# Kernel tuning notes

Measured on AMD Instinct MI355X. Metric: run time of the kernel, lower is better.

Reference implementation:

```python
import jax, jax.numpy as jnp
import numpy as np
from jax import lax

ALPHA = 4.0  # spikingjelly default sigmoid surrogate alpha

@jax.custom_vjp
def spike(x):
    return (x >= 0.0).astype(x.dtype)

def _spike_fwd(x):
    return spike(x), x

def _spike_bwd(x, g):
    s = jax.nn.sigmoid(ALPHA * x)
    return (g * ALPHA * s * (1.0 - s),)

spike.defvjp(_spike_fwd, _spike_bwd)

def lif(x_seq, v_th=1.0, tau=2.0):
    # MultiStepLIFNode, v_reset=0, detach_reset=True, hard reset.
    def step(v, xt):
        v = v + (xt - v) / tau            # neuronal charge
        s = spike(v - v_th)               # fire
        v = v * (1.0 - lax.stop_gradient(s))  # detached hard reset to 0
        return v, s
    _, out = lax.scan(step, jnp.zeros_like(x_seq[0]), x_seq)
    return out

def bn(x, g, b, m, var, eps=1e-5):
    # BatchNorm1d inference over channel axis 2 of (T,B,C,N)
    inv = g / jnp.sqrt(var + eps)
    return x * inv[None, None, :, None] + (b - m * inv)[None, None, :, None]

def setup_inputs() -> dict:
    T, B, C, N = 4, 8, 512, 1024
    key = jax.random.key(0)
    ks = jax.random.split(key, 24)
    def w(k):  # 1x1 conv weight (C_out, C_in)
        return jax.random.normal(k, (C, C), jnp.float32) * (C ** -0.5)
    def bn_params(k):
        k1, k2, k3 = jax.random.split(k, 3)
        g = 1.0 + 0.1 * jax.random.normal(k1, (C,), jnp.float32)
        b = 0.1 * jax.random.normal(k2, (C,), jnp.float32)
        m = 0.1 * jax.random.normal(k3, (C,), jnp.float32)
        v = 0.5 + jax.random.uniform(jax.random.fold_in(k, 7), (C,), jnp.float32)
        return g, b, m, v
    gq, bq, mq, vq = bn_params(ks[1])
    gk, bk, mk, vk = bn_params(ks[3])
    gv, bv, mv, vv = bn_params(ks[5])
    gp, bp, mp, vp = bn_params(ks[7])
    return {
        'x': jax.random.normal(ks[0], (T, B, C, N), jnp.float32),
        'res_attn': jnp.zeros((1,), jnp.float32),
        'wq': w(ks[10]), 'gq': gq, 'bq': bq, 'mq': mq, 'vq': vq,
        'wk': w(ks[11]), 'gk': gk, 'bk': bk, 'mk': mk, 'vk': vk,
        'wv': w(ks[12]), 'gv': gv, 'bv': bv, 'mv': mv, 'vv': vv,
        'wp': w(ks[13]), 'pb': 0.1 * jax.random.normal(ks[14], (C,), jnp.float32),
        'gp': gp, 'bp': bp, 'mp': mp, 'vp': vp,
    }

def reference(x, res_attn, wq, gq, bq, mq, vq, wk, gk, bk, mk, vk,
              wv, gv, bv, mv, vv, wp, pb, gp, bp, mp, vp):
    T, B, C, N = x.shape
    H = 8
    d = C // H
    scale = 0.125

    def branch(w_, g_, b_, m_, v_):
        y = jnp.einsum('oc,tbcn->tbon', w_, x)  # 1x1 conv
        return lif(bn(y, g_, b_, m_, v_))        # (T,B,C,N) spikes

    def heads(y):
        # (T,B,C,N) -> (T,B,H,N,d)
        return y.transpose(0, 1, 3, 2).reshape(T, B, N, H, d).transpose(0, 1, 3, 2, 4)

    q = heads(branch(wq, gq, bq, mq, vq))
    k = heads(branch(wk, gk, bk, mk, vk))
    v = heads(branch(wv, gv, bv, mv, vv))

    kv = jnp.einsum('tbhnd,tbhne->tbhde', k, v)           # k^T @ v
    a = jnp.einsum('tbhnd,tbhde->tbhne', q, kv) * scale   # q @ (k^T v)
    a = a.transpose(0, 1, 2, 4, 3).reshape(T, B, C, N)
    a = lif(a, v_th=0.5)                                   # attn_lif

    p = jnp.einsum('oc,tbcn->tbon', wp, a) + pb[None, None, :, None]
    out = lif(bn(p, gp, bp, mp, vp))
    return out, v
```

## Files before the change

kernel.cpp:

```cpp
#include <hip/hip_runtime.h>

#define TDIM 4
#define BDIM 8
#define CDIM 512
#define NDIM 1024
#define HDIM 8
#define DDIM 64
#define BCN  (BDIM*CDIM*NDIM)
#define TBCN ((size_t)TDIM*BCN)
#define WFRS 262144

typedef __attribute__((ext_vector_type(8))) short bf16x8;
typedef __attribute__((ext_vector_type(4))) float f32x4;
typedef unsigned long long u64;
typedef unsigned short ushort_t;

__device__ __forceinline__ unsigned short f2bf(float f) {
    unsigned int u = __float_as_uint(f);
    u = (u + 0x7FFFu + ((u >> 16) & 1u)) >> 16;
    return (unsigned short)u;
}
__device__ __forceinline__ float bf2f(unsigned short h) {
    return __uint_as_float(((unsigned int)h) << 16);
}

__global__ __launch_bounds__(256) void wsplit(
    const float* __restrict__ W, unsigned short* __restrict__ Wfr)
{
    const int idx = blockIdx.x * 256 + threadIdx.x;
    const int o = idx >> 9, c = idx & 511;
    const float v = W[idx];
    const unsigned short h1 = f2bf(v);
    const float r1 = v - bf2f(h1);
    const unsigned short h2 = f2bf(r1);
    const float r2 = r1 - bf2f(h2);
    const unsigned short h3 = f2bf(r2);
    const size_t fo = ((((size_t)(o >> 4)) * 16 + (c >> 5)) * 64 +
                       ((o & 15) | (((c >> 3) & 3) << 4))) * 8 + (c & 7);
    Wfr[fo]             = h1;
    Wfr[WFRS + fo]      = h2;
    Wfr[2 * WFRS + fo]  = h3;
}

__global__ __launch_bounds__(256) void xsplit(
    const float* __restrict__ X, unsigned short* __restrict__ xfr)
{
    const size_t idx = (size_t)blockIdx.x * 256 + threadIdx.x;
    const int n = (int)(idx & 1023);
    const int c = (int)(idx >> 10) & 511;
    const int tb = (int)(idx >> 19);
    const float v = X[idx];
    const unsigned short h1 = f2bf(v);
    const float r1 = v - bf2f(h1);
    const unsigned short h2 = f2bf(r1);
    const float r2 = r1 - bf2f(h2);
    const unsigned short h3 = f2bf(r2);
    const size_t fo = (((((size_t)tb * 64 + (n >> 4)) * 16 + (c >> 5)) * 64 +
                        ((n & 15) | (((c >> 3) & 3) << 4))) * 8) + (c & 7);
    xfr[fo]             = h1;
    xfr[TBCN + fo]      = h2;
    xfr[2 * TBCN + fo]  = h3;
}

template <int NSB>
__global__ __launch_bounds__(256, 2) void mfma_gemm(
    const unsigned short* __restrict__ Afr,
    const unsigned short* __restrict__ Bfr,
    float* __restrict__ Y,
    const float* __restrict__ bias)
{
    const int tb   = blockIdx.z;
    const int lane = threadIdx.x & 63;
    const int wv   = threadIdx.x >> 6;
    const int wo = wv >> 1, wn = wv & 1;
    const int ob_base = blockIdx.y * 8 + wo * 4;
    const int nb_base = blockIdx.x * 8 + wn * 4;

    f32x4 acc[4][4];
    #pragma unroll
    for (int m = 0; m < 4; ++m)
        #pragma unroll
        for (int n = 0; n < 4; ++n)
            acc[m][n] = (f32x4){0.f, 0.f, 0.f, 0.f};

    for (int kb = 0; kb < 16; ++kb) {
        bf16x8 bf[4][NSB];
        #pragma unroll
        for (int n = 0; n < 4; ++n) {
            const size_t bo = ((((size_t)tb * 64 + (nb_base + n)) * 16 + kb) * 64 + lane) * 8;
            #pragma unroll
            for (int s = 0; s < NSB; ++s)
                bf[n][s] = *(const bf16x8*)(Bfr + (size_t)s * TBCN + bo);
        }
        #pragma unroll
        for (int m = 0; m < 4; ++m) {
            const size_t ao = ((((size_t)(ob_base + m)) * 16 + kb) * 64 + lane) * 8;
            const bf16x8 a1 = *(const bf16x8*)(Afr + ao);
            const bf16x8 a2 = *(const bf16x8*)(Afr + WFRS + ao);
            const bf16x8 a3 = *(const bf16x8*)(Afr + 2 * WFRS + ao);
            #pragma unroll
            for (int n = 0; n < 4; ++n) {
                if (NSB == 3) {
                    acc[m][n] = __builtin_amdgcn_mfma_f32_16x16x32_bf16(a3, bf[n][0], acc[m][n], 0, 0, 0);
                    acc[m][n] = __builtin_amdgcn_mfma_f32_16x16x32_bf16(a1, bf[n][2], acc[m][n], 0, 0, 0);
                    acc[m][n] = __builtin_amdgcn_mfma_f32_16x16x32_bf16(a2, bf[n][1], acc[m][n], 0, 0, 0);
                    acc[m][n] = __builtin_amdgcn_mfma_f32_16x16x32_bf16(a2, bf[n][0], acc[m][n], 0, 0, 0);
                    acc[m][n] = __builtin_amdgcn_mfma_f32_16x16x32_bf16(a1, bf[n][1], acc[m][n], 0, 0, 0);
                    acc[m][n] = __builtin_amdgcn_mfma_f32_16x16x32_bf16(a1, bf[n][0], acc[m][n], 0, 0, 0);
                } else {
                    acc[m][n] = __builtin_amdgcn_mfma_f32_16x16x32_bf16(a3, bf[n][0], acc[m][n], 0, 0, 0);
                    acc[m][n] = __builtin_amdgcn_mfma_f32_16x16x32_bf16(a2, bf[n][0], acc[m][n], 0, 0, 0);
                    acc[m][n] = __builtin_amdgcn_mfma_f32_16x16x32_bf16(a1, bf[n][0], acc[m][n], 0, 0, 0);
                }
            }
        }
    }

    float* Yb = Y + (size_t)tb * CDIM * NDIM;
    #pragma unroll
    for (int m = 0; m < 4; ++m) {
        const int row0 = (ob_base + m) * 16 + (lane >> 4) * 4;
        #pragma unroll
        for (int r = 0; r < 4; ++r) {
            const int row = row0 + r;
            const float bvv = bias ? bias[row] : 0.0f;
            #pragma unroll
            for (int n = 0; n < 4; ++n) {
                const int col = (nb_base + n) * 16 + (lane & 15);
                Yb[(size_t)row * NDIM + col] = acc[m][n][r] + bvv;
            }
        }
    }
}

template <int OUT_MODE>
__global__ __launch_bounds__(256) void lif_bn(
    const float* __restrict__ Y,
    const float* __restrict__ g, const float* __restrict__ b,
    const float* __restrict__ m, const float* __restrict__ var,
    float vth,
    unsigned char* __restrict__ s8, float* __restrict__ sf,
    unsigned short* __restrict__ sfr,
    u64* __restrict__ bits)
{
    const int idx = blockIdx.x * 256 + threadIdx.x;
    const int c = (idx >> 10) & (CDIM - 1);
    float inv = 1.0f, beta = 0.0f;
    if (g) {
        const float iv = g[c] / sqrtf(var[c] + 1e-5f);
        inv = iv;
        beta = __fsub_rn(b[c], __fmul_rn(m[c], iv));
    }
    float v = 0.0f;
    #pragma unroll
    for (int t = 0; t < TDIM; ++t) {
        float x = Y[(size_t)t * BCN + idx];
        x = __fadd_rn(__fmul_rn(x, inv), beta);
        v = __fadd_rn(v, __fmul_rn(__fsub_rn(x, v), 0.5f));
        const float s = (v >= vth) ? 1.0f : 0.0f;
        v = v * (1.0f - s);
        if (OUT_MODE == 0) {
            if (s8) s8[(size_t)t * BCN + idx] = (unsigned char)s;
        } else if (OUT_MODE == 1) {
            sf[(size_t)t * BCN + idx] = s;
        } else {
            const int n = idx & 1023;
            const int bb = idx >> 19;
            const int tb = t * BDIM + bb;
            const size_t fo = (((((size_t)tb * 64 + (n >> 4)) * 16 + (c >> 5)) * 64 +
                                ((n & 15) | (((c >> 3) & 3) << 4))) * 8) + (c & 7);
            sfr[fo] = s != 0.0f ? (unsigned short)0x3F80 : (unsigned short)0;
        }
        if (bits) {
            u64 mask = __ballot(s != 0.0f);
            if ((threadIdx.x & 63) == 0)
                bits[((size_t)t * BCN + idx) >> 6] = mask;
        }
    }
}

__global__ __launch_bounds__(256) void v_transpose(
    const unsigned char* __restrict__ sv, float* __restrict__ out)
{
    const int tbh = blockIdx.y;
    const int h = tbh & 7, tb = tbh >> 3;
    const int n0 = blockIdx.x * 64;
    __shared__ unsigned char tile[64][65];
    const int tid = threadIdx.x;
    const int lane = tid & 63;
    for (int dd = tid >> 6; dd < 64; dd += 4)
        tile[dd][lane] = sv[((size_t)tb * CDIM + h * 64 + dd) * NDIM + n0 + lane];
    __syncthreads();
    for (int nn = tid >> 6; nn < 64; nn += 4)
        out[((size_t)tbh * NDIM + n0 + nn) * 64 + lane] = (float)tile[lane][nn];
}

__global__ __launch_bounds__(256) void kv_gemm(
    const u64* __restrict__ kb, const u64* __restrict__ vb,
    float* __restrict__ kv)
{
    const int tbh = blockIdx.x;
    const int h = tbh & 7, tb = tbh >> 3;
    __shared__ u64 sk[64][16], svv[64][16];
    const int tid = threadIdx.x;
    for (int i = tid; i < 1024; i += 256) {
        const int dd = i >> 4, w = i & 15;
        const size_t row = ((size_t)tb * CDIM + h * 64 + dd) * 16 + w;
        sk[dd][w] = kb[row];
        svv[dd][w] = vb[row];
    }
    __syncthreads();
    const int dd = tid >> 2, e0 = (tid & 3) * 16;
    #pragma unroll
    for (int j = 0; j < 16; ++j) {
        int acc = 0;
        #pragma unroll
        for (int w = 0; w < 16; ++w)
            acc += __popcll(sk[dd][w] & svv[e0 + j][w]);
        kv[((size_t)tbh * 64 + dd) * 64 + e0 + j] = (float)acc;
    }
}

__global__ __launch_bounds__(256) void a_gemm(
    const float* __restrict__ kv, const unsigned char* __restrict__ sq,
    float* __restrict__ Y)
{
    const int tbh = blockIdx.y;
    const int h = tbh & 7, tb = tbh >> 3;
    const int n0 = blockIdx.x * 64;
    __shared__ float skv[64][65];
    __shared__ float sqt[64][64];
    const int tid = threadIdx.x;
    for (int i = tid; i < 4096; i += 256)
        skv[i >> 6][i & 63] = kv[(size_t)tbh * 4096 + i];
    const int lane = tid & 63;
    for (int dd = tid >> 6; dd < 64; dd += 4)
        sqt[dd][lane] = (float)sq[((size_t)tb * CDIM + h * 64 + dd) * NDIM + n0 + lane];
    __syncthreads();

    const int tx = tid & 15, ty = tid >> 4;
    float acc[4][4] = {};
    #pragma unroll 8
    for (int dd = 0; dd < 64; ++dd) {
        float a_[4];
        #pragma unroll
        for (int i = 0; i < 4; ++i) a_[i] = skv[dd][ty * 4 + i];
        float4 b4 = *(float4*)&sqt[dd][tx * 4];
        float b_[4] = {b4.x, b4.y, b4.z, b4.w};
        #pragma unroll
        for (int i = 0; i < 4; ++i)
            #pragma unroll
            for (int j = 0; j < 4; ++j)
                acc[i][j] += a_[i] * b_[j];
    }
    #pragma unroll
    for (int i = 0; i < 4; ++i) {
        const int e = ty * 4 + i;
        float4 r = make_float4(acc[i][0] * 0.125f, acc[i][1] * 0.125f,
                               acc[i][2] * 0.125f, acc[i][3] * 0.125f);
        *(float4*)(Y + ((size_t)tb * CDIM + h * 64 + e) * NDIM + n0 + tx * 4) = r;
    }
}

extern "C" void kernel_launch(void* const* d_in, const int* in_sizes, int n_in,
                              void* d_out, int out_size, void* d_ws, size_t ws_size,
                              hipStream_t stream)
{
    const float* x  = (const float*)d_in[0];
    const float* wq = (const float*)d_in[2];
    const float* gq = (const float*)d_in[3];
    const float* bq = (const float*)d_in[4];
    const float* mq = (const float*)d_in[5];
    const float* vq = (const float*)d_in[6];
    const float* wk = (const float*)d_in[7];
    const float* gk = (const float*)d_in[8];
    const float* bk = (const float*)d_in[9];
    const float* mk = (const float*)d_in[10];
    const float* vk = (const float*)d_in[11];
    const float* wv = (const float*)d_in[12];
    const float* gv = (const float*)d_in[13];
    const float* bv = (const float*)d_in[14];
    const float* mv = (const float*)d_in[15];
    const float* vv = (const float*)d_in[16];
    const float* wp = (const float*)d_in[17];
    const float* pb = (const float*)d_in[18];
    const float* gp = (const float*)d_in[19];
    const float* bp = (const float*)d_in[20];
    const float* mp = (const float*)d_in[21];
    const float* vp = (const float*)d_in[22];
    (void)in_sizes; (void)n_in; (void)out_size; (void)ws_size;

    char* w = (char*)d_ws;
    float* Y = (float*)w;                     w += TBCN * 4;
    unsigned short* xfr = (unsigned short*)w; w += 3 * TBCN * 2;
    unsigned short* wfr = (unsigned short*)w; w += (size_t)4 * 3 * WFRS * 2;
    unsigned char* sq = (unsigned char*)w;    w += TBCN;
    unsigned char* sv = (unsigned char*)w;    w += TBCN;
    u64* kbb = (u64*)w;                       w += TBCN / 8;
    u64* vbb = (u64*)w;                       w += TBCN / 8;
    float* kvbuf = (float*)w;                 w += (size_t)256 * 4096 * 4;
    unsigned short* safr = xfr;

    float* out_spk = (float*)d_out;
    float* out_v   = (float*)d_out + TBCN;

    const dim3 blk(256);
    const dim3 gemmGrid(NDIM / 128, CDIM / 128, TDIM * BDIM);
    const int lifGrid = BCN / 256;

    wsplit<<<WFRS / 256, blk, 0, stream>>>(wq, wfr + (size_t)0 * 3 * WFRS);
    wsplit<<<WFRS / 256, blk, 0, stream>>>(wk, wfr + (size_t)1 * 3 * WFRS);
    wsplit<<<WFRS / 256, blk, 0, stream>>>(wv, wfr + (size_t)2 * 3 * WFRS);
    wsplit<<<WFRS / 256, blk, 0, stream>>>(wp, wfr + (size_t)3 * 3 * WFRS);
    xsplit<<<(int)(TBCN / 256), blk, 0, stream>>>(x, xfr);

    mfma_gemm<3><<<gemmGrid, blk, 0, stream>>>(wfr + (size_t)0 * 3 * WFRS, xfr, Y, nullptr);
    lif_bn<0><<<lifGrid, blk, 0, stream>>>(Y, gq, bq, mq, vq, 1.0f, sq, nullptr, nullptr, nullptr);
    mfma_gemm<3><<<gemmGrid, blk, 0, stream>>>(wfr + (size_t)1 * 3 * WFRS, xfr, Y, nullptr);
    lif_bn<0><<<lifGrid, blk, 0, stream>>>(Y, gk, bk, mk, vk, 1.0f, nullptr, nullptr, nullptr, kbb);
    mfma_gemm<3><<<gemmGrid, blk, 0, stream>>>(wfr + (size_t)2 * 3 * WFRS, xfr, Y, nullptr);
    lif_bn<0><<<lifGrid, blk, 0, stream>>>(Y, gv, bv, mv, vv, 1.0f, sv, nullptr, nullptr, vbb);
    v_transpose<<<dim3(NDIM / 64, TDIM * BDIM * HDIM), blk, 0, stream>>>(sv, out_v);
    kv_gemm<<<TDIM * BDIM * HDIM, blk, 0, stream>>>(kbb, vbb, kvbuf);
    a_gemm<<<dim3(NDIM / 64, TDIM * BDIM * HDIM), blk, 0, stream>>>(kvbuf, sq, Y);
    lif_bn<2><<<lifGrid, blk, 0, stream>>>(Y, nullptr, nullptr, nullptr, nullptr, 0.5f,
                                           nullptr, nullptr, safr, nullptr);
    mfma_gemm<1><<<gemmGrid, blk, 0, stream>>>(wfr + (size_t)3 * 3 * WFRS, safr, Y, pb);
    lif_bn<1><<<lifGrid, blk, 0, stream>>>(Y, gp, bp, mp, vp, 1.0f, nullptr, out_spk, nullptr, nullptr);
}
```

Before: 780.9 us.

## Double-buffer B fragment loads and interleave MFMA passes across independent accumulators

The split-bf16 GEMM loop now prefetches the next k-block's B fragments into a second register buffer while the current block is computed, so global load latency is hidden behind the MFMA chain. The MFMA order is also restructured so each split-product pass runs across all 16 accumulator tiles before the next pass starts. Consecutive MFMAs therefore no longer depend on the same accumulator. This doubles B-fragment register usage and loads all A fragments up front, which raises VGPR pressure and may lower occupancy or cause spills.

```diff
diff --git a/kernel.cpp b/kernel.cpp
--- a/kernel.cpp
+++ b/kernel.cpp
@@ -13,7 +13,6 @@
 typedef __attribute__((ext_vector_type(8))) short bf16x8;
 typedef __attribute__((ext_vector_type(4))) float f32x4;
 typedef unsigned long long u64;
-typedef unsigned short ushort_t;
 
 __device__ __forceinline__ unsigned short f2bf(float f) {
     unsigned int u = __float_as_uint(f);
@@ -83,37 +82,51 @@
         for (int n = 0; n < 4; ++n)
             acc[m][n] = (f32x4){0.f, 0.f, 0.f, 0.f};
 
-    for (int kb = 0; kb < 16; ++kb) {
-        bf16x8 bf[4][NSB];
+    constexpr int NPASS = (NSB == 3) ? 6 : 3;
+    constexpr int PA3[6] = {2, 0, 1, 1, 0, 0};
+    constexpr int PB3[6] = {0, 2, 1, 0, 1, 0};
+    constexpr int PA1[6] = {2, 1, 0, 0, 0, 0};
+
+    bf16x8 bufA[4][NSB], bufB[4][NSB];
+
+    auto loadB = [&](bf16x8 (&bb)[4][NSB], int kb) {
         #pragma unroll
         for (int n = 0; n < 4; ++n) {
             const size_t bo = ((((size_t)tb * 64 + (nb_base + n)) * 16 + kb) * 64 + lane) * 8;
             #pragma unroll
             for (int s = 0; s < NSB; ++s)
-                bf[n][s] = *(const bf16x8*)(Bfr + (size_t)s * TBCN + bo);
-        }
+                bb[n][s] = *(const bf16x8*)(Bfr + (size_t)s * TBCN + bo);
+        }
+    };
+
+    auto compute = [&](bf16x8 (&bb)[4][NSB], int kb) {
+        bf16x8 a[3][4];
         #pragma unroll
         for (int m = 0; m < 4; ++m) {
             const size_t ao = ((((size_t)(ob_base + m)) * 16 + kb) * 64 + lane) * 8;
-            const bf16x8 a1 = *(const bf16x8*)(Afr + ao);
-            const bf16x8 a2 = *(const bf16x8*)(Afr + WFRS + ao);
-            const bf16x8 a3 = *(const bf16x8*)(Afr + 2 * WFRS + ao);
+            a[0][m] = *(const bf16x8*)(Afr + ao);
+            a[1][m] = *(const bf16x8*)(Afr + WFRS + ao);
+            a[2][m] = *(const bf16x8*)(Afr + 2 * WFRS + ao);
+        }
+        #pragma unroll
+        for (int p = 0; p < NPASS; ++p) {
+            const int ai = (NSB == 3) ? PA3[p] : PA1[p];
+            const int bi = (NSB == 3) ? PB3[p] : 0;
             #pragma unroll
-            for (int n = 0; n < 4; ++n) {
-                if (NSB == 3) {
-                    acc[m][n] = __builtin_amdgcn_mfma_f32_16x16x32_bf16(a3, bf[n][0], acc[m][n], 0, 0, 0);
-                    acc[m][n] = __builtin_amdgcn_mfma_f32_16x16x32_bf16(a1, bf[n][2], acc[m][n], 0, 0, 0);
-                    acc[m][n] = __builtin_amdgcn_mfma_f32_16x16x32_bf16(a2, bf[n][1], acc[m][n], 0, 0, 0);
-                    acc[m][n] = __builtin_amdgcn_mfma_f32_16x16x32_bf16(a2, bf[n][0], acc[m][n], 0, 0, 0);
-                    acc[m][n] = __builtin_amdgcn_mfma_f32_16x16x32_bf16(a1, bf[n][1], acc[m][n], 0, 0, 0);
-                    acc[m][n] = __builtin_amdgcn_mfma_f32_16x16x32_bf16(a1, bf[n][0], acc[m][n], 0, 0, 0);
-                } else {
-                    acc[m][n] = __builtin_amdgcn_mfma_f32_16x16x32_bf16(a3, bf[n][0], acc[m][n], 0, 0, 0);
-                    acc[m][n] = __builtin_amdgcn_mfma_f32_16x16x32_bf16(a2, bf[n][0], acc[m][n], 0, 0, 0);
-                    acc[m][n] = __builtin_amdgcn_mfma_f32_16x16x32_bf16(a1, bf[n][0], acc[m][n], 0, 0, 0);
-                }
-            }
-        }
+            for (int m = 0; m < 4; ++m)
+                #pragma unroll
+                for (int n = 0; n < 4; ++n)
+                    acc[m][n] = __builtin_amdgcn_mfma_f32_16x16x32_bf16(
+                        a[ai][m], bb[n][bi], acc[m][n], 0, 0, 0);
+        }
+    };
+
+    loadB(bufA, 0);
+    for (int kb = 0; kb < 16; kb += 2) {
+        loadB(bufB, kb + 1);
+        compute(bufA, kb);
+        if (kb < 14) loadB(bufA, kb + 2);
+        compute(bufB, kb + 1);
     }
 
     float* Yb = Y + (size_t)tb * CDIM * NDIM;
```

After: 801.8 us. 1.03x slower.
